# Kernel tuning notes

Hardware: AMD Instinct MI355X
Metric: run time of the kernel (lower is better)

Reference implementation:

```python
import jax, jax.numpy as jnp
import numpy as np

N_NODES = 100000
N_EDGES = 1600000
F_IN, HID, N_CLS = 128, 128, 64


def setup_inputs() -> dict:
    key = jax.random.key(0)
    ks = jax.random.split(key, 9)
    x = jax.random.normal(ks[0], (N_NODES, F_IN), dtype=jnp.float32)
    edge_index = jax.random.randint(ks[1], (2, N_EDGES), 0, N_NODES, dtype=jnp.int64)
    edge_attr = jax.random.uniform(ks[2], (N_EDGES,), dtype=jnp.float32)
    def glorot(k, fi, fo):
        lim = (6.0 / (fi + fo)) ** 0.5
        return jax.random.uniform(k, (fi, fo), minval=-lim, maxval=lim, dtype=jnp.float32)
    return {
        "x": x, "edge_index": edge_index, "edge_attr": edge_attr,
        "W1": glorot(ks[3], F_IN, HID), "b1": jnp.zeros((HID,), jnp.float32),
        "W2": glorot(ks[4], HID, HID), "b2": jnp.zeros((HID,), jnp.float32),
        "W3": glorot(ks[5], HID, N_CLS), "b3": jnp.zeros((N_CLS,), jnp.float32),
    }


def reference(x, edge_index, edge_attr, W1, b1, W2, b2, W3, b3):
    N = x.shape[0]
    # PyG GCNConv: add self-loops with weight 1, symmetric normalization
    loop = jnp.arange(N, dtype=edge_index.dtype)
    src = jnp.concatenate([edge_index[0], loop])  # [E+N]
    dst = jnp.concatenate([edge_index[1], loop])
    w = jnp.concatenate([edge_attr, jnp.ones((N,), edge_attr.dtype)])
    deg = jax.ops.segment_sum(w, dst, num_segments=N)  # [N]
    dinv = jnp.where(deg > 0, deg ** -0.5, 0.0)
    norm = dinv[src] * w * dinv[dst]  # [E+N]

    def gcn_conv(h, W, b):
        h = h @ W                                 # [N, out]
        msg = norm[:, None] * h[src]              # [E+N, out] gather
        agg = jax.ops.segment_sum(msg, dst, num_segments=N)  # scatter-add
        return agg + b

    # dropout is identity in eval mode
    h = jax.nn.relu(gcn_conv(x, W1, b1))
    h = jax.nn.relu(gcn_conv(h, W2, b2))
    return gcn_conv(h, W3, b3)
```

## Files before the change

kernel.cpp:

```cpp
#include <hip/hip_runtime.h>
#include <hip/hip_fp16.h>


#define F_IN 128
#define HID  128
#define N_CLS 64

#define EDGE_CHUNK 8192
#define BCAP 6144

typedef _Float16 h8 __attribute__((ext_vector_type(8)));
typedef float f32x4 __attribute__((ext_vector_type(4)));


__global__ void k_zero(int* __restrict__ p, int n) {
    int i = blockIdx.x * blockDim.x + threadIdx.x;
    if (i < n) p[i] = 0;
}

__global__ void k_bscatter(const int* __restrict__ src, const int* __restrict__ dst,
                           const float* __restrict__ w, int* __restrict__ cursor,
                           int2* __restrict__ stage, int E) {
    __shared__ int lcnt[512];
    __shared__ int lbase[512];
    const int t = threadIdx.x;
    for (int i = t; i < 512; i += 256) lcnt[i] = 0;
    __syncthreads();
    const int base = blockIdx.x * EDGE_CHUNK;
    int d[32];
#pragma unroll
    for (int i = 0; i < 32; ++i) {
        int e = base + i * 256 + t;
        d[i] = (e < E) ? dst[e] : -1;
        if (d[i] >= 0) atomicAdd(&lcnt[d[i] >> 8], 1);
    }
    __syncthreads();
    for (int i = t; i < 512; i += 256) {
        int c = lcnt[i];
        lbase[i] = (c > 0) ? atomicAdd(&cursor[i], c) : 0;
        lcnt[i] = 0;
    }
    __syncthreads();
#pragma unroll
    for (int i = 0; i < 32; ++i) {
        int e = base + i * 256 + t;
        if (e >= E) continue;
        int dd = d[i];
        int b  = dd >> 8;
        int p  = lbase[b] + atomicAdd(&lcnt[b], 1);
        if (p < BCAP)
            stage[(size_t)b * BCAP + p] =
                make_int2(src[e] | ((dd & 255) << 20), __float_as_int(w[e]));
    }
}

__global__ void k_bscan(const int* __restrict__ cursor, int* __restrict__ bbase,
                        int NB, int E) {
    __shared__ int sh[512];
    const int t = threadIdx.x;
    sh[t] = (t < NB) ? cursor[t] : 0;
    __syncthreads();
    for (int off = 1; off < 512; off <<= 1) {
        int x = (t >= off) ? sh[t - off] : 0;
        __syncthreads();
        sh[t] += x;
        __syncthreads();
    }
    if (t < NB) bbase[t] = (t == 0) ? 0 : sh[t - 1];
    if (t == 0) bbase[NB] = E;
}

__global__ void k_bucket_csr(const int2* __restrict__ stage, const int* __restrict__ bbase,
                             int* __restrict__ row_ptr, int2* __restrict__ csr,
                             float* __restrict__ dinv, int n, int E) {
    __shared__ int   scn[256];
    __shared__ int   cur[256];
    __shared__ float degf[256];
    const int b = blockIdx.x, t = threadIdx.x;
    const int beg = bbase[b];
    const int cnt0 = bbase[b + 1] - beg;
    const int cnt  = (cnt0 < BCAP) ? cnt0 : BCAP;
    const int2* sl = stage + (size_t)b * BCAP;
    scn[t] = 0;
    degf[t] = 0.0f;
    __syncthreads();
    for (int j = t; j < cnt; j += 256)
        atomicAdd(&scn[sl[j].x >> 20], 1);
    __syncthreads();
    int own = scn[t];
    __syncthreads();
    for (int off = 1; off < 256; off <<= 1) {
        int x = (t >= off) ? scn[t - off] : 0;
        __syncthreads();
        scn[t] += x;
        __syncthreads();
    }
    const int excl = scn[t] - own;
    const int node = b * 256 + t;
    if (node < n) row_ptr[node] = beg + excl;
    cur[t] = excl;
    __syncthreads();
    for (int j = t; j < cnt; j += 256) {
        int2 s = sl[j];
        int dlow = s.x >> 20;
        float ww = __int_as_float(s.y);
        int pos = beg + atomicAdd(&cur[dlow], 1);
        csr[pos] = make_int2(s.x & 0xFFFFF, s.y);
        atomicAdd(&degf[dlow], ww);
    }
    __syncthreads();
    if (node < n) dinv[node] = rsqrtf(1.0f + degf[t]);
    if (b == 0 && t == 0) row_ptr[n] = E;
}

__global__ void k_nw(int2* __restrict__ csr, const float* __restrict__ dinv, int E) {
    int j = blockIdx.x * blockDim.x + threadIdx.x;
    if (j < E) {
        int2 e = csr[j];
        e.y = __float_as_int(dinv[e.x] * __int_as_float(e.y));
        csr[j] = e;
    }
}


__global__ void k_wcvt(const float* __restrict__ W1, const float* __restrict__ W2,
                       const float* __restrict__ W3,
                       _Float16* __restrict__ T1, _Float16* __restrict__ T2,
                       _Float16* __restrict__ T3) {
    int id = blockIdx.x * blockDim.x + threadIdx.x;
    if (id < 16384) {
        int n = id >> 7, k = id & 127;
        T1[n * 128 + k] = (_Float16)W1[k * 128 + n];
    } else if (id < 32768) {
        int i = id - 16384;
        int n = i >> 7, k = i & 127;
        T2[n * 128 + k] = (_Float16)W2[k * 128 + n];
    } else if (id < 40960) {
        int i = id - 32768;
        int n = i >> 7, k = i & 127;
        T3[n * 128 + k] = (_Float16)W3[k * 64 + n];
    }
}


template <int BN, typename TA>
__launch_bounds__(256)
__global__ void k_mm_mfma(const TA* __restrict__ A, const _Float16* __restrict__ WT,
                          __half* __restrict__ C, int nrows) {
    constexpr int K   = 128;
    constexpr int NCT = BN / 16;
    constexpr int KP  = K + 8;
    constexpr int CP  = BN + 8;
    __shared__ _Float16 lw[BN * KP];
    __shared__ _Float16 lc[64 * CP];
    const int tid  = threadIdx.x;
    const int wave = tid >> 6;
    const int lane = tid & 63;
    const int bm0  = blockIdx.x * 64;

    for (int c = tid; c < BN * 16; c += 256) {
        int n = c >> 4, k = (c & 15) * 8;
        *(h8*)&lw[n * KP + k] = *(const h8*)&WT[n * 128 + k];
    }
    __syncthreads();

    f32x4 acc[NCT];
#pragma unroll
    for (int ct = 0; ct < NCT; ++ct)
#pragma unroll
        for (int i = 0; i < 4; ++i) acc[ct][i] = 0.0f;

    const int row = bm0 + wave * 16 + (lane & 15);
    const int kb  = (lane >> 4) * 8;
    const bool rok = row < nrows;

#pragma unroll
    for (int kk = 0; kk < 4; ++kk) {
        const int k0 = kk * 32 + kb;
        h8 va;
        if (rok) {
            if constexpr (__is_same(TA, float)) {
                float4 f0 = *(const float4*)&A[(size_t)row * K + k0];
                float4 f1 = *(const float4*)&A[(size_t)row * K + k0 + 4];
                va[0] = (_Float16)f0.x; va[1] = (_Float16)f0.y;
                va[2] = (_Float16)f0.z; va[3] = (_Float16)f0.w;
                va[4] = (_Float16)f1.x; va[5] = (_Float16)f1.y;
                va[6] = (_Float16)f1.z; va[7] = (_Float16)f1.w;
            } else {
                va = *(const h8*)&A[(size_t)row * K + k0];
            }
        } else {
#pragma unroll
            for (int i = 0; i < 8; ++i) va[i] = (_Float16)0.0f;
        }
#pragma unroll
        for (int ct = 0; ct < NCT; ++ct) {
            h8 vb = *(const h8*)&lw[(ct * 16 + (lane & 15)) * KP + k0];
            acc[ct] = __builtin_amdgcn_mfma_f32_16x16x32_f16(va, vb, acc[ct], 0, 0, 0);
        }
    }

#pragma unroll
    for (int ct = 0; ct < NCT; ++ct)
#pragma unroll
        for (int r = 0; r < 4; ++r)
            lc[(wave * 16 + (lane >> 4) * 4 + r) * CP + ct * 16 + (lane & 15)] =
                (_Float16)acc[ct][r];
    __syncthreads();

    constexpr int NCH = (64 * BN / 8) / 256;
#pragma unroll
    for (int i = 0; i < NCH; ++i) {
        int c = i * 256 + tid;
        int r = c / (BN / 8), col = (c % (BN / 8)) * 8;
        int grow = bm0 + r;
        if (grow < nrows)
            *(h8*)&C[(size_t)grow * BN + col] = *(const h8*)&lc[r * CP + col];
    }
}


template <int NCOL, bool RELU, typename TO>
__launch_bounds__(256)
__global__ void k_agg(const __half* __restrict__ XW, const int* __restrict__ row_ptr,
                      const int2* __restrict__ csr,
                      const float* __restrict__ dinv, const float* __restrict__ bias,
                      TO* __restrict__ out, int n) {
    constexpr int PER = NCOL / 64;
    int wid  = (blockIdx.x * blockDim.x + threadIdx.x) >> 6;
    int lane = threadIdx.x & 63;
    if (wid >= n) return;
    const int node = __builtin_amdgcn_readfirstlane(wid);
    const float dn  = dinv[node];
    const int  beg  = row_ptr[node];
    const int  end  = row_ptr[node + 1];

    float a0, a1 = 0.0f;
    {
        if (PER == 2) {
            __half2 hv = *(const __half2*)&XW[(size_t)node * NCOL + lane * 2];
            a0 = dn * __low2float(hv); a1 = dn * __high2float(hv);
        } else {
            a0 = dn * __half2float(XW[(size_t)node * NCOL + lane]);
        }
    }

    int j = beg;
    for (; j + 4 <= end; j += 4) {
        int2 e0 = csr[j + 0], e1 = csr[j + 1], e2 = csr[j + 2], e3 = csr[j + 3];
        float w0 = __int_as_float(e0.y), w1 = __int_as_float(e1.y);
        float w2 = __int_as_float(e2.y), w3 = __int_as_float(e3.y);
        if (PER == 2) {
            __half2 v0 = *(const __half2*)&XW[(size_t)e0.x * NCOL + lane * 2];
            __half2 v1 = *(const __half2*)&XW[(size_t)e1.x * NCOL + lane * 2];
            __half2 v2 = *(const __half2*)&XW[(size_t)e2.x * NCOL + lane * 2];
            __half2 v3 = *(const __half2*)&XW[(size_t)e3.x * NCOL + lane * 2];
            a0 = fmaf(w0, __low2float(v0), a0); a1 = fmaf(w0, __high2float(v0), a1);
            a0 = fmaf(w1, __low2float(v1), a0); a1 = fmaf(w1, __high2float(v1), a1);
            a0 = fmaf(w2, __low2float(v2), a0); a1 = fmaf(w2, __high2float(v2), a1);
            a0 = fmaf(w3, __low2float(v3), a0); a1 = fmaf(w3, __high2float(v3), a1);
        } else {
            float v0 = __half2float(XW[(size_t)e0.x * NCOL + lane]);
            float v1 = __half2float(XW[(size_t)e1.x * NCOL + lane]);
            float v2 = __half2float(XW[(size_t)e2.x * NCOL + lane]);
            float v3 = __half2float(XW[(size_t)e3.x * NCOL + lane]);
            a0 = fmaf(w0, v0, a0);
            a0 = fmaf(w1, v1, a0);
            a0 = fmaf(w2, v2, a0);
            a0 = fmaf(w3, v3, a0);
        }
    }
    for (; j < end; ++j) {
        int2 e = csr[j];
        float nw = __int_as_float(e.y);
        if (PER == 2) {
            __half2 v = *(const __half2*)&XW[(size_t)e.x * NCOL + lane * 2];
            a0 = fmaf(nw, __low2float(v), a0); a1 = fmaf(nw, __high2float(v), a1);
        } else {
            a0 = fmaf(nw, __half2float(XW[(size_t)e.x * NCOL + lane]), a0);
        }
    }

    if (PER == 2) {
        a0 = fmaf(dn, a0, bias[lane * 2 + 0]);
        a1 = fmaf(dn, a1, bias[lane * 2 + 1]);
        if (RELU) { a0 = fmaxf(a0, 0.0f); a1 = fmaxf(a1, 0.0f); }
        if constexpr (__is_same(TO, float)) {
            *(float2*)&out[(size_t)node * NCOL + lane * 2] = make_float2(a0, a1);
        } else {
            *(__half2*)&out[(size_t)node * NCOL + lane * 2] = __floats2half2_rn(a0, a1);
        }
    } else {
        a0 = fmaf(dn, a0, bias[lane]);
        if (RELU) a0 = fmaxf(a0, 0.0f);
        if constexpr (__is_same(TO, float)) {
            out[(size_t)node * NCOL + lane] = a0;
        } else {
            out[(size_t)node * NCOL + lane] = __float2half(a0);
        }
    }
}


extern "C" void kernel_launch(void* const* d_in, const int* in_sizes, int n_in,
                              void* d_out, int out_size, void* d_ws, size_t ws_size,
                              hipStream_t stream) {
    const float* x  = (const float*)d_in[0];
    const int*   ei = (const int*)d_in[1];
    const float* ea = (const float*)d_in[2];
    const float* W1 = (const float*)d_in[3];
    const float* b1 = (const float*)d_in[4];
    const float* W2 = (const float*)d_in[5];
    const float* b2 = (const float*)d_in[6];
    const float* W3 = (const float*)d_in[7];
    const float* b3 = (const float*)d_in[8];

    const int N = in_sizes[0] / F_IN;
    const int E = in_sizes[1] / 2;
    const int* src = ei;
    const int* dst = ei + E;
    const int NB = (N + 255) / 256;

    char* ws = (char*)d_ws;
    size_t off = 0;
    auto alloc = [&](size_t bytes) -> void* {
        void* p = ws + off;
        off += (bytes + 255) & ~(size_t)255;
        return p;
    };
    __half*    bufH    = (__half*)   alloc((size_t)N * HID * sizeof(__half));
    __half*    bufH2   = (__half*)   alloc((size_t)N * HID * sizeof(__half));
    float*     dinv    = (float*)    alloc((size_t)N * sizeof(float));
    int*       row_ptr = (int*)      alloc((size_t)(N + 1) * sizeof(int));
    int2*      csr     = (int2*)     alloc((size_t)E * sizeof(int2));
    int2*      stage   = (int2*)     alloc((size_t)NB * BCAP * sizeof(int2));
    int*       cursor  = (int*)      alloc((size_t)NB * sizeof(int));
    int*       bbase   = (int*)      alloc((size_t)(NB + 1) * sizeof(int));
    _Float16*  W1T     = (_Float16*) alloc((size_t)128 * 128 * sizeof(_Float16));
    _Float16*  W2T     = (_Float16*) alloc((size_t)128 * 128 * sizeof(_Float16));
    _Float16*  W3T     = (_Float16*) alloc((size_t)64 * 128 * sizeof(_Float16));
    (void)ws_size;

    const int BLK = 256;
    const int gE  = (E + BLK - 1) / BLK;
    const int nEB = (E + EDGE_CHUNK - 1) / EDGE_CHUNK;

    k_wcvt<<<(40960 + BLK - 1) / BLK, BLK, 0, stream>>>(W1, W2, W3, W1T, W2T, W3T);
    k_zero<<<(NB + 255) / 256, BLK, 0, stream>>>(cursor, NB);
    k_bscatter<<<nEB, BLK, 0, stream>>>(src, dst, ea, cursor, stage, E);
    k_bscan<<<1, 512, 0, stream>>>(cursor, bbase, NB, E);
    k_bucket_csr<<<NB, BLK, 0, stream>>>(stage, bbase, row_ptr, csr, dinv, N, E);
    k_nw<<<gE, BLK, 0, stream>>>(csr, dinv, E);

    const int gMM = (N + 63) / 64;
    const int gAG = (N + 3) / 4;

    k_mm_mfma<HID, float><<<gMM, BLK, 0, stream>>>(x, W1T, bufH, N);
    k_agg<HID, true, __half><<<gAG, BLK, 0, stream>>>(bufH, row_ptr, csr, dinv, b1, bufH2, N);
    k_mm_mfma<HID, __half><<<gMM, BLK, 0, stream>>>(bufH2, W2T, bufH, N);
    k_agg<HID, true, __half><<<gAG, BLK, 0, stream>>>(bufH, row_ptr, csr, dinv, b2, bufH2, N);
    k_mm_mfma<N_CLS, __half><<<gMM, BLK, 0, stream>>>(bufH2, W3T, bufH, N);
    k_agg<N_CLS, false, float><<<gAG, BLK, 0, stream>>>(bufH, row_ptr, csr, dinv, b3, (float*)d_out, N);
}
```

Before: 293.8 us.

## Fold cursor zeroing, scan and norm weighting into fewer preprocessing kernels

Cursor zeroing moves into the weight-conversion kernel. The bucket scan and degree computation are merged into a new slab-degree kernel. The source-side dinv scaling now happens inside the CSR build instead of a separate pass over all edges. This removes two or three launches and one full read-modify-write pass over the CSR array. In exchange, the stage slabs are read one extra time and block 0 does the scan serially after its degree work.

```diff
diff --git a/kernel.cpp b/kernel.cpp
--- a/kernel.cpp
+++ b/kernel.cpp
@@ -13,121 +13,13 @@
 typedef float f32x4 __attribute__((ext_vector_type(4)));
 
 
-__global__ void k_zero(int* __restrict__ p, int n) {
-    int i = blockIdx.x * blockDim.x + threadIdx.x;
-    if (i < n) p[i] = 0;
-}
-
-__global__ void k_bscatter(const int* __restrict__ src, const int* __restrict__ dst,
-                           const float* __restrict__ w, int* __restrict__ cursor,
-                           int2* __restrict__ stage, int E) {
-    __shared__ int lcnt[512];
-    __shared__ int lbase[512];
-    const int t = threadIdx.x;
-    for (int i = t; i < 512; i += 256) lcnt[i] = 0;
-    __syncthreads();
-    const int base = blockIdx.x * EDGE_CHUNK;
-    int d[32];
-#pragma unroll
-    for (int i = 0; i < 32; ++i) {
-        int e = base + i * 256 + t;
-        d[i] = (e < E) ? dst[e] : -1;
-        if (d[i] >= 0) atomicAdd(&lcnt[d[i] >> 8], 1);
-    }
-    __syncthreads();
-    for (int i = t; i < 512; i += 256) {
-        int c = lcnt[i];
-        lbase[i] = (c > 0) ? atomicAdd(&cursor[i], c) : 0;
-        lcnt[i] = 0;
-    }
-    __syncthreads();
-#pragma unroll
-    for (int i = 0; i < 32; ++i) {
-        int e = base + i * 256 + t;
-        if (e >= E) continue;
-        int dd = d[i];
-        int b  = dd >> 8;
-        int p  = lbase[b] + atomicAdd(&lcnt[b], 1);
-        if (p < BCAP)
-            stage[(size_t)b * BCAP + p] =
-                make_int2(src[e] | ((dd & 255) << 20), __float_as_int(w[e]));
-    }
-}
-
-__global__ void k_bscan(const int* __restrict__ cursor, int* __restrict__ bbase,
-                        int NB, int E) {
-    __shared__ int sh[512];
-    const int t = threadIdx.x;
-    sh[t] = (t < NB) ? cursor[t] : 0;
-    __syncthreads();
-    for (int off = 1; off < 512; off <<= 1) {
-        int x = (t >= off) ? sh[t - off] : 0;
-        __syncthreads();
-        sh[t] += x;
-        __syncthreads();
-    }
-    if (t < NB) bbase[t] = (t == 0) ? 0 : sh[t - 1];
-    if (t == 0) bbase[NB] = E;
-}
-
-__global__ void k_bucket_csr(const int2* __restrict__ stage, const int* __restrict__ bbase,
-                             int* __restrict__ row_ptr, int2* __restrict__ csr,
-                             float* __restrict__ dinv, int n, int E) {
-    __shared__ int   scn[256];
-    __shared__ int   cur[256];
-    __shared__ float degf[256];
-    const int b = blockIdx.x, t = threadIdx.x;
-    const int beg = bbase[b];
-    const int cnt0 = bbase[b + 1] - beg;
-    const int cnt  = (cnt0 < BCAP) ? cnt0 : BCAP;
-    const int2* sl = stage + (size_t)b * BCAP;
-    scn[t] = 0;
-    degf[t] = 0.0f;
-    __syncthreads();
-    for (int j = t; j < cnt; j += 256)
-        atomicAdd(&scn[sl[j].x >> 20], 1);
-    __syncthreads();
-    int own = scn[t];
-    __syncthreads();
-    for (int off = 1; off < 256; off <<= 1) {
-        int x = (t >= off) ? scn[t - off] : 0;
-        __syncthreads();
-        scn[t] += x;
-        __syncthreads();
-    }
-    const int excl = scn[t] - own;
-    const int node = b * 256 + t;
-    if (node < n) row_ptr[node] = beg + excl;
-    cur[t] = excl;
-    __syncthreads();
-    for (int j = t; j < cnt; j += 256) {
-        int2 s = sl[j];
-        int dlow = s.x >> 20;
-        float ww = __int_as_float(s.y);
-        int pos = beg + atomicAdd(&cur[dlow], 1);
-        csr[pos] = make_int2(s.x & 0xFFFFF, s.y);
-        atomicAdd(&degf[dlow], ww);
-    }
-    __syncthreads();
-    if (node < n) dinv[node] = rsqrtf(1.0f + degf[t]);
-    if (b == 0 && t == 0) row_ptr[n] = E;
-}
-
-__global__ void k_nw(int2* __restrict__ csr, const float* __restrict__ dinv, int E) {
-    int j = blockIdx.x * blockDim.x + threadIdx.x;
-    if (j < E) {
-        int2 e = csr[j];
-        e.y = __float_as_int(dinv[e.x] * __int_as_float(e.y));
-        csr[j] = e;
-    }
-}
-
-
 __global__ void k_wcvt(const float* __restrict__ W1, const float* __restrict__ W2,
                        const float* __restrict__ W3,
                        _Float16* __restrict__ T1, _Float16* __restrict__ T2,
-                       _Float16* __restrict__ T3) {
+                       _Float16* __restrict__ T3,
+                       int* __restrict__ cursor, int NB) {
     int id = blockIdx.x * blockDim.x + threadIdx.x;
+    if (id < NB) cursor[id] = 0;
     if (id < 16384) {
         int n = id >> 7, k = id & 127;
         T1[n * 128 + k] = (_Float16)W1[k * 128 + n];
@@ -140,6 +32,115 @@
         int n = i >> 7, k = i & 127;
         T3[n * 128 + k] = (_Float16)W3[k * 64 + n];
     }
+}
+
+
+__global__ void k_bscatter(const int* __restrict__ src, const int* __restrict__ dst,
+                           const float* __restrict__ w, int* __restrict__ cursor,
+                           int2* __restrict__ stage, int E) {
+    __shared__ int lcnt[512];
+    __shared__ int lbase[512];
+    const int t = threadIdx.x;
+    for (int i = t; i < 512; i += 256) lcnt[i] = 0;
+    __syncthreads();
+    const int base = blockIdx.x * EDGE_CHUNK;
+    int d[32];
+#pragma unroll
+    for (int i = 0; i < 32; ++i) {
+        int e = base + i * 256 + t;
+        d[i] = (e < E) ? dst[e] : -1;
+        if (d[i] >= 0) atomicAdd(&lcnt[d[i] >> 8], 1);
+    }
+    __syncthreads();
+    for (int i = t; i < 512; i += 256) {
+        int c = lcnt[i];
+        lbase[i] = (c > 0) ? atomicAdd(&cursor[i], c) : 0;
+        lcnt[i] = 0;
+    }
+    __syncthreads();
+#pragma unroll
+    for (int i = 0; i < 32; ++i) {
+        int e = base + i * 256 + t;
+        if (e >= E) continue;
+        int dd = d[i];
+        int b  = dd >> 8;
+        int p  = lbase[b] + atomicAdd(&lcnt[b], 1);
+        if (p < BCAP)
+            stage[(size_t)b * BCAP + p] =
+                make_int2(src[e] | ((dd & 255) << 20), __float_as_int(w[e]));
+    }
+}
+
+__global__ void k_slabdeg(const int2* __restrict__ stage, const int* __restrict__ cursor,
+                          float* __restrict__ dinv, int* __restrict__ bbase,
+                          int n, int NB, int E) {
+    __shared__ float degf[256];
+    __shared__ int   sh[512];
+    const int b = blockIdx.x, t = threadIdx.x;
+    if (t < 256) degf[t] = 0.0f;
+    __syncthreads();
+    const int cnt0 = cursor[b];
+    const int cnt  = (cnt0 < BCAP) ? cnt0 : BCAP;
+    const int2* sl = stage + (size_t)b * BCAP;
+    for (int j = t; j < cnt; j += 512) {
+        int2 s = sl[j];
+        atomicAdd(&degf[s.x >> 20], __int_as_float(s.y));
+    }
+    __syncthreads();
+    const int node = b * 256 + t;
+    if (t < 256 && node < n) dinv[node] = rsqrtf(1.0f + degf[t]);
+
+    if (b == 0) {
+        sh[t] = (t < NB) ? min(cursor[t], BCAP) : 0;
+        __syncthreads();
+        for (int off = 1; off < 512; off <<= 1) {
+            int x = (t >= off) ? sh[t - off] : 0;
+            __syncthreads();
+            sh[t] += x;
+            __syncthreads();
+        }
+        if (t < NB) bbase[t] = (t == 0) ? 0 : sh[t - 1];
+        if (t == 0) bbase[NB] = E;
+    }
+}
+
+__global__ void k_bucket_csr(const int2* __restrict__ stage, const int* __restrict__ bbase,
+                             const float* __restrict__ dinv,
+                             int* __restrict__ row_ptr, int2* __restrict__ csr,
+                             int n, int E) {
+    __shared__ int scn[256];
+    __shared__ int cur[256];
+    const int b = blockIdx.x, t = threadIdx.x;
+    const int beg = bbase[b];
+    const int cnt = bbase[b + 1] - beg;
+    const int2* sl = stage + (size_t)b * BCAP;
+    scn[t] = 0;
+    __syncthreads();
+    for (int j = t; j < cnt; j += 256)
+        atomicAdd(&scn[sl[j].x >> 20], 1);
+    __syncthreads();
+    int own = scn[t];
+    __syncthreads();
+    for (int off = 1; off < 256; off <<= 1) {
+        int x = (t >= off) ? scn[t - off] : 0;
+        __syncthreads();
+        scn[t] += x;
+        __syncthreads();
+    }
+    const int excl = scn[t] - own;
+    const int node = b * 256 + t;
+    if (node < n) row_ptr[node] = beg + excl;
+    cur[t] = excl;
+    __syncthreads();
+    for (int j = t; j < cnt; j += 256) {
+        int2 s = sl[j];
+        int dlow = s.x >> 20;
+        int srcid = s.x & 0xFFFFF;
+        float nw = dinv[srcid] * __int_as_float(s.y);
+        int pos = beg + atomicAdd(&cur[dlow], 1);
+        csr[pos] = make_int2(srcid, __float_as_int(nw));
+    }
+    if (b == 0 && t == 0) row_ptr[n] = E;
 }
 
 
@@ -342,15 +343,13 @@
     (void)ws_size;
 
     const int BLK = 256;
-    const int gE  = (E + BLK - 1) / BLK;
     const int nEB = (E + EDGE_CHUNK - 1) / EDGE_CHUNK;
 
-    k_wcvt<<<(40960 + BLK - 1) / BLK, BLK, 0, stream>>>(W1, W2, W3, W1T, W2T, W3T);
-    k_zero<<<(NB + 255) / 256, BLK, 0, stream>>>(cursor, NB);
+    k_wcvt<<<(40960 + BLK - 1) / BLK, BLK, 0, stream>>>(W1, W2, W3, W1T, W2T, W3T,
+                                                        cursor, NB);
     k_bscatter<<<nEB, BLK, 0, stream>>>(src, dst, ea, cursor, stage, E);
-    k_bscan<<<1, 512, 0, stream>>>(cursor, bbase, NB, E);
-    k_bucket_csr<<<NB, BLK, 0, stream>>>(stage, bbase, row_ptr, csr, dinv, N, E);
-    k_nw<<<gE, BLK, 0, stream>>>(csr, dinv, E);
+    k_slabdeg<<<NB, 512, 0, stream>>>(stage, cursor, dinv, bbase, N, NB, E);
+    k_bucket_csr<<<NB, BLK, 0, stream>>>(stage, bbase, dinv, row_ptr, csr, N, E);
 
     const int gMM = (N + 63) / 64;
     const int gAG = (N + 3) / 4;
```

Result: no change. 293.5 us (-0.1%).
